# Performance work log

Hardware: AMD Instinct MI355X
Metric: run time of the kernel (lower is better)

The kernel has to match this reference:

```python
import jax, jax.numpy as jnp
import numpy as np

STD = 1.0  # components_std from cfg
LOG_2PI = float(np.log(2.0 * np.pi))


def setup_inputs() -> dict:
    key = jax.random.key(0)
    k1, k2, k3 = jax.random.split(key, 3)
    B, S, D, K = 256, 1024, 32, 512
    x = jax.random.normal(k1, (B, S, D), dtype=jnp.float32)
    logits = jax.random.normal(k2, (B, K), dtype=jnp.float32)
    # xavier_normal_ init on (K, D): std = sqrt(2 / (K + D))
    means = jax.random.normal(k3, (K, D), dtype=jnp.float32) * np.sqrt(2.0 / (K + D))
    return {"x": x, "logits": logits, "means": means}


def reference(x, logits, means):
    # x: [B, S, D], logits: [B, K], means: [K, D]
    D = x.shape[-1]
    log_mix = jax.nn.log_softmax(logits, axis=-1)  # [B, K] Categorical log-probs
    # squared distance ||x - mu||^2 via expansion (avoids [B,S,K,D] intermediate)
    x2 = jnp.sum(x * x, axis=-1)          # [B, S]
    m2 = jnp.sum(means * means, axis=-1)  # [K]
    xm = jnp.einsum('bsd,kd->bsk', x, means)  # [B, S, K]
    sq = x2[..., None] - 2.0 * xm + m2        # [B, S, K]
    inv_var = 1.0 / (STD * STD)
    log_norm = D * (jnp.log(jnp.float32(STD)) + 0.5 * LOG_2PI)
    comp_logpdf = -0.5 * inv_var * sq - log_norm  # [B, S, K] Independent-Normal logpdf
    # mixture log_prob = logsumexp over components; NLL = negative
    nll = -jax.nn.logsumexp(log_mix[:, None, :] + comp_logpdf, axis=-1)  # [B, S]
    return nll
```

## Files before the change

### kernel.cpp

```cpp
#include <hip/hip_runtime.h>
#include <math.h>

constexpr int Bc = 256, Sc = 1024, Dc = 32, Kc = 512;
constexpr int ST = 128;
constexpr float LOG2E    = 1.4426950408889634f;
constexpr float LN2      = 0.6931471805599453f;
constexpr float LOG_NORM = 29.40603306051f;

typedef __attribute__((ext_vector_type(8))) short          bf16x8;
typedef __attribute__((ext_vector_type(8))) unsigned short u16x8;
typedef __attribute__((ext_vector_type(4))) float          f32x4;

#if __has_builtin(__builtin_amdgcn_exp2f)
#define EXP2F(v) __builtin_amdgcn_exp2f(v)
#else
#define EXP2F(v) exp2f(v)
#endif
#if __has_builtin(__builtin_amdgcn_logf)
#define LOG2F(v) __builtin_amdgcn_logf(v)
#else
#define LOG2F(v) log2f(v)
#endif

__device__ __forceinline__ unsigned short f2bf(float f) {
    unsigned u = __float_as_uint(f);
    u += 0x7fff + ((u >> 16) & 1);
    return (unsigned short)(u >> 16);
}

__device__ __forceinline__ int swz(int row, int chunk) {
    return row * 32 + ((chunk ^ ((row >> 1) & 3)) << 3);
}

__global__ __launch_bounds__(256)
void gm_nll_mfma(const float* __restrict__ x, const float* __restrict__ logits,
                 const float* __restrict__ means, float* __restrict__ out)
{
    __shared__ unsigned short mlds[Kc * 32];
    __shared__ unsigned short xlds[ST * 32];
    __shared__ float a2s[Kc];
    __shared__ float x2p[256];
    __shared__ float red[8];

    const int tid  = threadIdx.x;
    const int lane = tid & 63;
    const int wid  = tid >> 6;
    const int b    = blockIdx.x >> 3;
    const int s0   = (blockIdx.x & 7) * ST;

    const float l0 = logits[b * Kc + 2 * tid];
    const float l1 = logits[b * Kc + 2 * tid + 1];
    float mx = fmaxf(l0, l1);
    #pragma unroll
    for (int off = 32; off >= 1; off >>= 1) mx = fmaxf(mx, __shfl_xor(mx, off));
    if (lane == 0) red[wid] = mx;
    __syncthreads();
    mx = fmaxf(fmaxf(red[0], red[1]), fmaxf(red[2], red[3]));
    float sm = EXP2F((l0 - mx) * LOG2E) + EXP2F((l1 - mx) * LOG2E);
    #pragma unroll
    for (int off = 32; off >= 1; off >>= 1) sm += __shfl_xor(sm, off);
    if (lane == 0) red[4 + wid] = sm;
    __syncthreads();
    sm = red[4] + red[5] + red[6] + red[7];
    const float lse = mx + LN2 * LOG2F(sm);

    {
        const float4* mp4 = (const float4*)means + (size_t)tid * 16;
        #pragma unroll
        for (int rr = 0; rr < 2; ++rr) {
            const int row = 2 * tid + rr;
            float m2 = 0.f;
            #pragma unroll
            for (int c = 0; c < 4; ++c) {
                float4 v0 = mp4[rr * 8 + 2 * c];
                float4 v1 = mp4[rr * 8 + 2 * c + 1];
                m2 += v0.x*v0.x + v0.y*v0.y + v0.z*v0.z + v0.w*v0.w
                    + v1.x*v1.x + v1.y*v1.y + v1.z*v1.z + v1.w*v1.w;
                u16x8 pk;
                pk[0]=f2bf(v0.x); pk[1]=f2bf(v0.y); pk[2]=f2bf(v0.z); pk[3]=f2bf(v0.w);
                pk[4]=f2bf(v1.x); pk[5]=f2bf(v1.y); pk[6]=f2bf(v1.z); pk[7]=f2bf(v1.w);
                *(u16x8*)&mlds[swz(row, c)] = pk;
            }
            const float lg = (rr == 0) ? l0 : l1;
            a2s[row] = (lg - lse - 0.5f * m2) * LOG2E;
        }
    }

    {
        const int row = tid >> 1, h = tid & 1;
        const float4* xp4 = (const float4*)(x + ((size_t)b * Sc + s0 + row) * Dc) + h * 4;
        float s2 = 0.f;
        #pragma unroll
        for (int j = 0; j < 2; ++j) {
            float4 v0 = xp4[2 * j];
            float4 v1 = xp4[2 * j + 1];
            s2 += v0.x*v0.x + v0.y*v0.y + v0.z*v0.z + v0.w*v0.w
                + v1.x*v1.x + v1.y*v1.y + v1.z*v1.z + v1.w*v1.w;
            u16x8 pk;
            pk[0]=f2bf(v0.x*LOG2E); pk[1]=f2bf(v0.y*LOG2E);
            pk[2]=f2bf(v0.z*LOG2E); pk[3]=f2bf(v0.w*LOG2E);
            pk[4]=f2bf(v1.x*LOG2E); pk[5]=f2bf(v1.y*LOG2E);
            pk[6]=f2bf(v1.z*LOG2E); pk[7]=f2bf(v1.w*LOG2E);
            *(u16x8*)&xlds[swz(row, 2 * h + j)] = pk;
        }
        x2p[tid] = s2;
    }
    __syncthreads();

    const int q  = lane >> 4;
    const int ln = lane & 15;
    const int rw = wid * 32;

    const bf16x8 a0 = *(const bf16x8*)&xlds[swz(rw + ln, q)];
    const bf16x8 a1 = *(const bf16x8*)&xlds[swz(rw + 16 + ln, q)];

    float acc0[4] = {0.f, 0.f, 0.f, 0.f};
    float acc1[4] = {0.f, 0.f, 0.f, 0.f};

    #pragma unroll 4
    for (int kt = 0; kt < 32; ++kt) {
        const int krow = kt * 16 + ln;
        const bf16x8 bfr = *(const bf16x8*)&mlds[swz(krow, q)];
        const float a2v = a2s[krow];
        f32x4 c; c[0] = a2v; c[1] = a2v; c[2] = a2v; c[3] = a2v;
        f32x4 d0 = __builtin_amdgcn_mfma_f32_16x16x32_bf16(a0, bfr, c, 0, 0, 0);
        f32x4 d1 = __builtin_amdgcn_mfma_f32_16x16x32_bf16(a1, bfr, c, 0, 0, 0);
        #pragma unroll
        for (int r = 0; r < 4; ++r) {
            acc0[r] += EXP2F(d0[r]);
            acc1[r] += EXP2F(d1[r]);
        }
    }

    #pragma unroll
    for (int r = 0; r < 4; ++r) {
        float v0 = acc0[r], v1 = acc1[r];
        v0 += __shfl_xor(v0, 1); v0 += __shfl_xor(v0, 2);
        v0 += __shfl_xor(v0, 4); v0 += __shfl_xor(v0, 8);
        v1 += __shfl_xor(v1, 1); v1 += __shfl_xor(v1, 2);
        v1 += __shfl_xor(v1, 4); v1 += __shfl_xor(v1, 8);
        if (ln == 0) {
            const int r0 = rw + q * 4 + r;
            const int r1 = r0 + 16;
            out[(size_t)b * Sc + s0 + r0] =
                0.5f * (x2p[2 * r0] + x2p[2 * r0 + 1]) + LOG_NORM - LN2 * LOG2F(v0);
            out[(size_t)b * Sc + s0 + r1] =
                0.5f * (x2p[2 * r1] + x2p[2 * r1 + 1]) + LOG_NORM - LN2 * LOG2F(v1);
        }
    }
}

extern "C" void kernel_launch(void* const* d_in, const int* in_sizes, int n_in,
                              void* d_out, int out_size, void* d_ws, size_t ws_size,
                              hipStream_t stream) {
    const float* x      = (const float*)d_in[0];
    const float* logits = (const float*)d_in[1];
    const float* means  = (const float*)d_in[2];
    float* out = (float*)d_out;
    (void)in_sizes; (void)n_in; (void)out_size; (void)d_ws; (void)ws_size;

    dim3 grid(Bc * (Sc / ST)), block(256);
    hipLaunchKernelGGL(gm_nll_mfma, grid, block, 0, stream, x, logits, means, out);
}
```

Baseline: 100.2 us.

## Split mixture-weight and bf16-means prep into a separate kernel ahead of main

Adds a prep kernel that computes the log-softmax, the per-component norm term and exponentiated mixture weights once per batch, and converts the means to bf16 once into workspace. The main kernel now just copies the pre-converted means into LDS, loads x straight into MFMA operand registers, and applies the weight as a multiply after the exponential instead of a bias in the accumulator. This removes the per-block recomputation of the softmax and the float-to-bf16 conversion of all means, which was repeated across 2048 blocks. The cost is a second launch, a dependency on the workspace buffer, and an unswizzled LDS layout that may cause bank conflicts.

```diff
diff --git a/kernel.cpp b/kernel.cpp
--- a/kernel.cpp
+++ b/kernel.cpp
@@ -28,28 +28,18 @@
     return (unsigned short)(u >> 16);
 }
 
-__device__ __forceinline__ int swz(int row, int chunk) {
-    return row * 32 + ((chunk ^ ((row >> 1) & 3)) << 3);
-}
-
 __global__ __launch_bounds__(256)
-void gm_nll_mfma(const float* __restrict__ x, const float* __restrict__ logits,
-                 const float* __restrict__ means, float* __restrict__ out)
+void gm_prep(const float* __restrict__ logits, const float* __restrict__ means,
+             float* __restrict__ wbuf, unsigned short* __restrict__ mbf)
 {
-    __shared__ unsigned short mlds[Kc * 32];
-    __shared__ unsigned short xlds[ST * 32];
-    __shared__ float a2s[Kc];
-    __shared__ float x2p[256];
     __shared__ float red[8];
-
     const int tid  = threadIdx.x;
     const int lane = tid & 63;
     const int wid  = tid >> 6;
-    const int b    = blockIdx.x >> 3;
-    const int s0   = (blockIdx.x & 7) * ST;
+    const int b    = blockIdx.x;
 
-    const float l0 = logits[b * Kc + 2 * tid];
-    const float l1 = logits[b * Kc + 2 * tid + 1];
+    const float l0 = logits[b * Kc + tid];
+    const float l1 = logits[b * Kc + tid + 256];
     float mx = fmaxf(l0, l1);
     #pragma unroll
     for (int off = 32; off >= 1; off >>= 1) mx = fmaxf(mx, __shfl_xor(mx, off));
@@ -64,88 +54,110 @@
     sm = red[4] + red[5] + red[6] + red[7];
     const float lse = mx + LN2 * LOG2F(sm);
 
-    {
-        const float4* mp4 = (const float4*)means + (size_t)tid * 16;
+    #pragma unroll
+    for (int rr = 0; rr < 2; ++rr) {
+        const int k = tid + rr * 256;
+        const float4* mp = (const float4*)(means + (size_t)k * Dc);
+        float m2 = 0.f;
         #pragma unroll
-        for (int rr = 0; rr < 2; ++rr) {
-            const int row = 2 * tid + rr;
-            float m2 = 0.f;
-            #pragma unroll
-            for (int c = 0; c < 4; ++c) {
-                float4 v0 = mp4[rr * 8 + 2 * c];
-                float4 v1 = mp4[rr * 8 + 2 * c + 1];
-                m2 += v0.x*v0.x + v0.y*v0.y + v0.z*v0.z + v0.w*v0.w
-                    + v1.x*v1.x + v1.y*v1.y + v1.z*v1.z + v1.w*v1.w;
-                u16x8 pk;
-                pk[0]=f2bf(v0.x); pk[1]=f2bf(v0.y); pk[2]=f2bf(v0.z); pk[3]=f2bf(v0.w);
-                pk[4]=f2bf(v1.x); pk[5]=f2bf(v1.y); pk[6]=f2bf(v1.z); pk[7]=f2bf(v1.w);
-                *(u16x8*)&mlds[swz(row, c)] = pk;
-            }
-            const float lg = (rr == 0) ? l0 : l1;
-            a2s[row] = (lg - lse - 0.5f * m2) * LOG2E;
+        for (int i = 0; i < 8; ++i) {
+            float4 v = mp[i];
+            m2 += v.x*v.x + v.y*v.y + v.z*v.z + v.w*v.w;
         }
+        const float lg = (rr == 0) ? l0 : l1;
+        wbuf[(size_t)b * Kc + k] = EXP2F((lg - lse - 0.5f * m2) * LOG2E);
     }
 
+    if (tid < 64) {
+        const int row = 2 * b + (tid >> 5);
+        const int col = tid & 31;
+        mbf[row * 32 + col] = f2bf(means[(size_t)row * 32 + col]);
+    }
+}
+
+__global__ __launch_bounds__(256)
+void gm_main(const float* __restrict__ x, const float* __restrict__ wbuf,
+             const unsigned short* __restrict__ mbf, float* __restrict__ out)
+{
+    __shared__ unsigned short mlds[Kc * 32];
+    __shared__ float x2p[ST];
+
+    const int tid  = threadIdx.x;
+    const int lane = tid & 63;
+    const int wid  = tid >> 6;
+    const int b    = blockIdx.x >> 3;
+    const int s0   = (blockIdx.x & 7) * ST;
+    const int q    = lane >> 4;
+    const int ln   = lane & 15;
+    const int rw   = wid * 32;
+
     {
-        const int row = tid >> 1, h = tid & 1;
-        const float4* xp4 = (const float4*)(x + ((size_t)b * Sc + s0 + row) * Dc) + h * 4;
-        float s2 = 0.f;
+        const u16x8* src = (const u16x8*)mbf;
+        u16x8*       dst = (u16x8*)mlds;
         #pragma unroll
-        for (int j = 0; j < 2; ++j) {
-            float4 v0 = xp4[2 * j];
-            float4 v1 = xp4[2 * j + 1];
-            s2 += v0.x*v0.x + v0.y*v0.y + v0.z*v0.z + v0.w*v0.w
-                + v1.x*v1.x + v1.y*v1.y + v1.z*v1.z + v1.w*v1.w;
-            u16x8 pk;
-            pk[0]=f2bf(v0.x*LOG2E); pk[1]=f2bf(v0.y*LOG2E);
-            pk[2]=f2bf(v0.z*LOG2E); pk[3]=f2bf(v0.w*LOG2E);
-            pk[4]=f2bf(v1.x*LOG2E); pk[5]=f2bf(v1.y*LOG2E);
-            pk[6]=f2bf(v1.z*LOG2E); pk[7]=f2bf(v1.w*LOG2E);
-            *(u16x8*)&xlds[swz(row, 2 * h + j)] = pk;
-        }
-        x2p[tid] = s2;
+        for (int j = 0; j < 8; ++j) dst[tid + j * 256] = src[tid + j * 256];
+    }
+
+    const int row0 = rw + ln, row1 = row0 + 16;
+    const float4* xp0 = (const float4*)(x + ((size_t)b * Sc + s0 + row0) * Dc) + q * 2;
+    const float4* xp1 = (const float4*)(x + ((size_t)b * Sc + s0 + row1) * Dc) + q * 2;
+    float4 v0 = xp0[0], v1 = xp0[1];
+    float4 u0 = xp1[0], u1 = xp1[1];
+
+    bf16x8 a0, a1;
+    a0[0]=(short)f2bf(v0.x*LOG2E); a0[1]=(short)f2bf(v0.y*LOG2E);
+    a0[2]=(short)f2bf(v0.z*LOG2E); a0[3]=(short)f2bf(v0.w*LOG2E);
+    a0[4]=(short)f2bf(v1.x*LOG2E); a0[5]=(short)f2bf(v1.y*LOG2E);
+    a0[6]=(short)f2bf(v1.z*LOG2E); a0[7]=(short)f2bf(v1.w*LOG2E);
+    a1[0]=(short)f2bf(u0.x*LOG2E); a1[1]=(short)f2bf(u0.y*LOG2E);
+    a1[2]=(short)f2bf(u0.z*LOG2E); a1[3]=(short)f2bf(u0.w*LOG2E);
+    a1[4]=(short)f2bf(u1.x*LOG2E); a1[5]=(short)f2bf(u1.y*LOG2E);
+    a1[6]=(short)f2bf(u1.z*LOG2E); a1[7]=(short)f2bf(u1.w*LOG2E);
+
+    float p0 = v0.x*v0.x + v0.y*v0.y + v0.z*v0.z + v0.w*v0.w
+             + v1.x*v1.x + v1.y*v1.y + v1.z*v1.z + v1.w*v1.w;
+    float p1 = u0.x*u0.x + u0.y*u0.y + u0.z*u0.z + u0.w*u0.w
+             + u1.x*u1.x + u1.y*u1.y + u1.z*u1.z + u1.w*u1.w;
+    p0 += __shfl_xor(p0, 16); p0 += __shfl_xor(p0, 32);
+    p1 += __shfl_xor(p1, 16); p1 += __shfl_xor(p1, 32);
+    if (q == 0) { x2p[row0] = p0; x2p[row1] = p1; }
+
+    float wreg[32];
+    {
+        const float* wrow = wbuf + (size_t)b * Kc + ln;
+        #pragma unroll
+        for (int kt = 0; kt < 32; ++kt) wreg[kt] = wrow[kt * 16];
     }
     __syncthreads();
 
-    const int q  = lane >> 4;
-    const int ln = lane & 15;
-    const int rw = wid * 32;
-
-    const bf16x8 a0 = *(const bf16x8*)&xlds[swz(rw + ln, q)];
-    const bf16x8 a1 = *(const bf16x8*)&xlds[swz(rw + 16 + ln, q)];
-
+    const f32x4 zero = {0.f, 0.f, 0.f, 0.f};
     float acc0[4] = {0.f, 0.f, 0.f, 0.f};
     float acc1[4] = {0.f, 0.f, 0.f, 0.f};
 
-    #pragma unroll 4
+    #pragma unroll
     for (int kt = 0; kt < 32; ++kt) {
-        const int krow = kt * 16 + ln;
-        const bf16x8 bfr = *(const bf16x8*)&mlds[swz(krow, q)];
-        const float a2v = a2s[krow];
-        f32x4 c; c[0] = a2v; c[1] = a2v; c[2] = a2v; c[3] = a2v;
-        f32x4 d0 = __builtin_amdgcn_mfma_f32_16x16x32_bf16(a0, bfr, c, 0, 0, 0);
-        f32x4 d1 = __builtin_amdgcn_mfma_f32_16x16x32_bf16(a1, bfr, c, 0, 0, 0);
+        const bf16x8 bfr = *(const bf16x8*)&mlds[(kt * 16 + ln) * 32 + q * 8];
+        f32x4 d0 = __builtin_amdgcn_mfma_f32_16x16x32_bf16(a0, bfr, zero, 0, 0, 0);
+        f32x4 d1 = __builtin_amdgcn_mfma_f32_16x16x32_bf16(a1, bfr, zero, 0, 0, 0);
         #pragma unroll
         for (int r = 0; r < 4; ++r) {
-            acc0[r] += EXP2F(d0[r]);
-            acc1[r] += EXP2F(d1[r]);
+            acc0[r] = fmaf(wreg[kt], EXP2F(d0[r]), acc0[r]);
+            acc1[r] = fmaf(wreg[kt], EXP2F(d1[r]), acc1[r]);
         }
     }
 
     #pragma unroll
     for (int r = 0; r < 4; ++r) {
-        float v0 = acc0[r], v1 = acc1[r];
-        v0 += __shfl_xor(v0, 1); v0 += __shfl_xor(v0, 2);
-        v0 += __shfl_xor(v0, 4); v0 += __shfl_xor(v0, 8);
-        v1 += __shfl_xor(v1, 1); v1 += __shfl_xor(v1, 2);
-        v1 += __shfl_xor(v1, 4); v1 += __shfl_xor(v1, 8);
+        float s0v = acc0[r], s1v = acc1[r];
+        s0v += __shfl_xor(s0v, 1); s0v += __shfl_xor(s0v, 2);
+        s0v += __shfl_xor(s0v, 4); s0v += __shfl_xor(s0v, 8);
+        s1v += __shfl_xor(s1v, 1); s1v += __shfl_xor(s1v, 2);
+        s1v += __shfl_xor(s1v, 4); s1v += __shfl_xor(s1v, 8);
         if (ln == 0) {
             const int r0 = rw + q * 4 + r;
             const int r1 = r0 + 16;
-            out[(size_t)b * Sc + s0 + r0] =
-                0.5f * (x2p[2 * r0] + x2p[2 * r0 + 1]) + LOG_NORM - LN2 * LOG2F(v0);
-            out[(size_t)b * Sc + s0 + r1] =
-                0.5f * (x2p[2 * r1] + x2p[2 * r1 + 1]) + LOG_NORM - LN2 * LOG2F(v1);
+            out[(size_t)b * Sc + s0 + r0] = 0.5f * x2p[r0] + LOG_NORM - LN2 * LOG2F(s0v);
+            out[(size_t)b * Sc + s0 + r1] = 0.5f * x2p[r1] + LOG_NORM - LN2 * LOG2F(s1v);
         }
     }
 }
@@ -157,8 +169,13 @@
     const float* logits = (const float*)d_in[1];
     const float* means  = (const float*)d_in[2];
     float* out = (float*)d_out;
-    (void)in_sizes; (void)n_in; (void)out_size; (void)d_ws; (void)ws_size;
+    (void)in_sizes; (void)n_in; (void)out_size; (void)ws_size;
 
-    dim3 grid(Bc * (Sc / ST)), block(256);
-    hipLaunchKernelGGL(gm_nll_mfma, grid, block, 0, stream, x, logits, means, out);
+    unsigned short* mbf  = (unsigned short*)d_ws;
+    float*          wbuf = (float*)((char*)d_ws + 32768);
+
+    hipLaunchKernelGGL(gm_prep, dim3(Bc), dim3(256), 0, stream,
+                       logits, means, wbuf, mbf);
+    hipLaunchKernelGGL(gm_main, dim3(Bc * (Sc / ST)), dim3(256), 0, stream,
+                       x, wbuf, mbf, out);
 }
```

Result: slower. 122.8 us (+22.5%).
